# Optimization experiments

Measured on AMD Instinct MI355X. Metric: run time of the kernel, lower is better.

## Reference

```python
import jax, jax.numpy as jnp
import numpy as np

NV, C, ED, V, D, KS = 14, 2, 32, 3, 16, 3   # num_vars, codebook, embed_dim, views, depth, kernel
K_STATES = C ** NV                          # 16384 combinatorial states
B = 32


def _all_idcs():
    # itertools.product(range(C), repeat=NV) order: first variable varies slowest
    s = np.arange(K_STATES)
    pw = C ** np.arange(NV - 1, -1, -1)
    return (s[:, None] // pw[None, :]) % C  # (K, NV) int


def _convT(h, w, b):
    # torch ConvTranspose2d (stride=1, pad=0) == full conv with spatially-flipped kernel, in/out swapped
    wt = jnp.transpose(jnp.flip(w, (2, 3)), (1, 0, 2, 3))  # (out,in,k,k)
    y = jax.lax.conv_general_dilated(h, wt, (1, 1), [(KS - 1, KS - 1)] * 2,
                                     dimension_numbers=('NCHW', 'OIHW', 'NCHW'))
    return y + b[None, :, None, None]


def _decoder(z_flat, lw, lb, w1, b1, w2, b2, w3, b3):
    h = (z_flat @ lw + lb).reshape(-1, 4 * D, 1, 1)          # (K, 64, 1, 1)
    h = jax.nn.elu(_convT(h, w1, b1))                        # (K, 32, 3, 3)
    h = jax.nn.elu(_convT(h, w2, b2))                        # (K, 16, 5, 5)
    h = _convT(h, w3, b3)                                    # (K, 1, 7, 7)
    return h[:, 0]                                           # (K, 7, 7)


def setup_inputs() -> dict:
    key = jax.random.key(0)
    ks = jax.random.split(key, 6)
    sc = jnp.float32(0.05)
    return {
        'x': jax.random.normal(ks[0], (B, V, 7, 7), jnp.float32),
        'latent_embedding': jax.random.normal(ks[1], (NV, C, ED), jnp.float32),
        'lin_w': jax.random.normal(ks[2], (V, NV * ED, 4 * D), jnp.float32) * sc,
        'lin_b': jnp.zeros((V, 4 * D), jnp.float32),
        'w1': jax.random.normal(ks[3], (V, 4 * D, 2 * D, KS, KS), jnp.float32) * sc,
        'b1': jnp.zeros((V, 2 * D), jnp.float32),
        'w2': jax.random.normal(ks[4], (V, 2 * D, D, KS, KS), jnp.float32) * sc,
        'b2': jnp.zeros((V, D), jnp.float32),
        'w3': jax.random.normal(ks[5], (V, D, 1, KS, KS), jnp.float32) * sc,
        'b3': jnp.zeros((V, 1), jnp.float32),
    }


def reference(x, latent_embedding, lin_w, lin_b, w1, b1, w2, b2, w3, b3):
    idcs = jnp.asarray(_all_idcs())                                   # (K, NV) const
    z = latent_embedding[jnp.arange(NV)[None, :], idcs]               # (K, NV, ED)
    zf = z.reshape(K_STATES, NV * ED)
    means = jax.vmap(_decoder, in_axes=(None, 0, 0, 0, 0, 0, 0, 0, 0))(
        zf, lin_w, lin_b, w1, b1, w2, b2, w3, b3)                     # (V, K, 7, 7)
    means = jnp.transpose(means, (1, 0, 2, 3))                        # (K, V, 7, 7)
    # obs_logits: -0.5 * sum((means[None] - x[:, None])**2) over (h, w)
    return -0.5 * jnp.sum((means[None] - x[:, None]) ** 2, axis=(-2, -1))  # (B, K, V)
```

## Files before the change

kernel.cpp:

```cpp
#include <hip/hip_runtime.h>
#include <math.h>

#define NVARS 14
#define EDIM 32
#define VMIX 3
#define KSTATES 16384
#define BATCH 32

#define WS_DSWZ_B  32768
#define WS_W2SWZ_B (WS_DSWZ_B + 55296)
#define WS_W3SWZ_B (WS_W2SWZ_B + 718848)

#define H1S 296
#define H2S 420
#define MS  72

typedef __attribute__((ext_vector_type(8))) short bf16x8;
typedef __attribute__((ext_vector_type(4))) float f32x4;
typedef __attribute__((ext_vector_type(2))) unsigned int u32x2;

static __device__ inline unsigned short f2bf(float f) {
    unsigned u = __float_as_uint(f);
    u += 0x7FFFu + ((u >> 16) & 1u);
    return (unsigned short)(u >> 16);
}
static __device__ inline unsigned cvtpk(float lo, float hi) {
    unsigned r;
    asm("v_cvt_pk_bf16_f32 %0, %1, %2" : "=v"(r) : "v"(lo), "v"(hi));
    return r;
}
static __device__ inline float elu(float x) {
    return x > 0.f ? x : (__expf(x) - 1.f);
}

__global__ __launch_bounds__(320) void pre_kernel(const float* __restrict__ emb,
                                                  const float* __restrict__ lin_w,
                                                  const float* __restrict__ lin_b,
                                                  const float* __restrict__ b1,
                                                  const float* __restrict__ w1,
                                                  const float* __restrict__ w2,
                                                  const float* __restrict__ w3,
                                                  float* __restrict__ ws) {
    int blk = blockIdx.x;
    int tid = threadIdx.x;
    char* wsb = (char*)ws;
    unsigned short* dmat = (unsigned short*)(wsb + WS_DSWZ_B);
    __shared__ float sP[128];
    __shared__ float sQ[64];

    if (blk < 172) {
        int g2 = blk * 320 + tid;
        if (g2 >= 54912) return;
        bf16x8 o8;
        if (g2 < 44928) {
            int h = g2;
            int v = h / 14976;
            int r = h % 14976;
            int kt = r / 1664;
            int r2 = r % 1664;
            int nt = r2 / 64, l = r2 % 64;
            int n = nt * 16 + (l & 15);
            int kbase = kt * 32 + ((l >> 4) & 3) * 8;
            #pragma unroll
            for (int j = 0; j < 8; ++j) {
                int k = kbase + j;
                float val = 0.f;
                if (n < 400) {
                    int i = k / 9, p = k % 9;
                    int py = p / 3, px = p % 3;
                    int o = n / 25, q = n % 25;
                    int qy = q / 5, qx = q % 5;
                    int ty = qy - py, tx = qx - px;
                    if (ty >= 0 && ty < 3 && tx >= 0 && tx < 3)
                        val = w2[((size_t)(v * 32 + i) * 16 + o) * 9 + ty * 3 + tx];
                }
                o8[j] = (short)f2bf(val);
            }
        } else {
            int h = g2 - 44928;
            int v = h / 3328;
            int r = h % 3328;
            int kt = r / 256;
            int r2 = r % 256;
            int nt = r2 / 64, l = r2 % 64;
            int n = nt * 16 + (l & 15);
            int kbase = kt * 32 + ((l >> 4) & 3) * 8;
            #pragma unroll
            for (int j = 0; j < 8; ++j) {
                int k = kbase + j;
                float val = 0.f;
                if (k < 400 && n < 49) {
                    int o = k / 25, q = k % 25;
                    int qy = q / 5, qx = q % 5;
                    int py = n / 7, px = n % 7;
                    int ty = py - qy, tx = px - qx;
                    if (ty >= 0 && ty < 3 && tx >= 0 && tx < 3)
                        val = w3[(size_t)(v * 16 + o) * 9 + ty * 3 + tx];
                }
                o8[j] = (short)f2bf(val);
            }
        }
        *(bf16x8*)(wsb + WS_DSWZ_B + ((size_t)g2 + 3456) * 16) = o8;
        return;
    }

    if (blk < 214) {
        int b = blk - 172;
        int v = b / 14;
        int k = b % 14;
        if (tid < 128) {
            int c = tid >> 6, i = tid & 63;
            const float* e = emb + (k * 2 + c) * EDIM;
            const float* lw = lin_w + ((size_t)v * 448 + k * 32) * 64 + i;
            float a0 = 0.f, a1 = 0.f;
            #pragma unroll
            for (int e2 = 0; e2 < 32; e2 += 2) {
                a0 = fmaf(e[e2], lw[e2 * 64], a0);
                a1 = fmaf(e[e2 + 1], lw[(e2 + 1) * 64], a1);
            }
            sP[tid] = a0 + a1;
        }
        __syncthreads();
        if (tid < 64) sQ[tid] = sP[64 + tid] - sP[tid];
        __syncthreads();
        if (tid < 288) {
            int n = tid;
            const float* w1v = w1 + (size_t)v * 64 * 288 + n;
            float a0 = 0.f, a1 = 0.f;
            #pragma unroll
            for (int i = 0; i < 64; i += 2) {
                a0 = fmaf(sQ[i], w1v[i * 288], a0);
                a1 = fmaf(sQ[i + 1], w1v[(i + 1) * 288], a1);
            }
            int nt = n >> 4;
            int l = (n & 15) | ((k >> 3) << 4);
            dmat[((size_t)(v * 18 + nt) * 64 + l) * 8 + (k & 7)] = f2bf(a0 + a1);
        }
        return;
    }

    {
        int v = blk - 214;
        for (int t = tid; t < 9216; t += 320) {
            int j3 = t & 7;
            int l = (t >> 3) & 63;
            int k2 = ((l >> 4) << 3) | j3;
            if (k2 >= 15) dmat[(size_t)v * 9216 + t] = 0;
        }
        if (tid < 128) {
            int half = tid >> 6, i = tid & 63;
            float a0 = 0.f, a1 = 0.f;
            for (int n2 = half * 7; n2 < half * 7 + 7; ++n2) {
                const float* e = emb + (n2 * 2) * EDIM;
                const float* lw = lin_w + ((size_t)v * 448 + n2 * 32) * 64 + i;
                #pragma unroll
                for (int e2 = 0; e2 < 32; e2 += 2) {
                    a0 = fmaf(e[e2], lw[e2 * 64], a0);
                    a1 = fmaf(e[e2 + 1], lw[(e2 + 1) * 64], a1);
                }
            }
            sP[tid] = a0 + a1;
        }
        __syncthreads();
        if (tid < 64) sQ[tid] = lin_b[v * 64 + tid] + sP[tid] + sP[64 + tid];
        __syncthreads();
        if (tid < 288) {
            int n = tid;
            const float* w1v = w1 + (size_t)v * 64 * 288 + n;
            float a0 = b1[v * 32 + n / 9], a1 = 0.f;
            #pragma unroll
            for (int i = 0; i < 64; i += 2) {
                a0 = fmaf(sQ[i], w1v[i * 288], a0);
                a1 = fmaf(sQ[i + 1], w1v[(i + 1) * 288], a1);
            }
            int nt = n >> 4;
            int l = (n & 15) | 16;
            dmat[((size_t)(v * 18 + nt) * 64 + l) * 8 + 6] = f2bf(a0 + a1);
        }
    }
}

__global__ __launch_bounds__(512, 4) void emission_main(const float* __restrict__ x,
                                                        const float* __restrict__ b2,
                                                        const float* __restrict__ b3p,
                                                        const float* __restrict__ ws,
                                                        float* __restrict__ out) {
    int bid = blockIdx.x;
    int group = bid / 24;
    int j24 = bid % 24;
    int v = j24 >> 3;
    int chunk = group * 8 + (j24 & 7);
    int tid = threadIdx.x;
    int w = tid >> 6;
    int l = tid & 63;
    int quad = l >> 4;
    int lc = l & 15;
    const char* wsb = (const char*)ws;

    __shared__ __align__(16) unsigned short uni[64 * H2S];
    __shared__ float sMsq[64];
    __shared__ float sXsq[32];
    __shared__ float sB2[16];

    if (tid < 16) sB2[tid] = b2[v * 16 + tid];
    if (tid < 64) sMsq[tid] = 0.f;
    if (tid >= 64 && tid < 96) {
        int b = tid - 64;
        const float* xb = x + (size_t)(b * 3 + v) * 49;
        float s = 0.f;
        #pragma unroll
        for (int p = 0; p < 49; ++p) s = fmaf(xb[p], xb[p], s);
        sXsq[b] = s;
    }

    int mt0 = w & 3;
    {
        int nh = w >> 2;
        int sg = chunk * 64 + mt0 * 16 + lc;
        bf16x8 abits;
        #pragma unroll
        for (int j = 0; j < 8; ++j) {
            int k = quad * 8 + j;
            unsigned short u = 0;
            if (k < 14) u = ((sg >> (13 - k)) & 1) ? 0x3F80 : 0;
            else if (k == 14) u = 0x3F80;
            abits[j] = (short)u;
        }
        const bf16x8* dsw = (const bf16x8*)(wsb + WS_DSWZ_B) + (size_t)v * 18 * 64;
        #pragma unroll 3
        for (int i = 0; i < 9; ++i) {
            int nt = nh * 9 + i;
            bf16x8 afrag = dsw[nt * 64 + l];
            f32x4 d = {0.f, 0.f, 0.f, 0.f};
            d = __builtin_amdgcn_mfma_f32_16x16x32_bf16(afrag, abits, d, 0, 0, 0);
            unsigned lo = cvtpk(elu(d[0]), elu(d[1]));
            unsigned hi = cvtpk(elu(d[2]), elu(d[3]));
            *(u32x2*)&uni[(mt0 * 16 + lc) * H1S + nt * 16 + quad * 4] = (u32x2){lo, hi};
        }
    }
    __syncthreads();

    int ncnt = (w == 0) ? 4 : 3;
    int n0 = (w == 0) ? 0 : 1 + 3 * w;
    f32x4 acc[4][4];
    #pragma unroll
    for (int mt = 0; mt < 4; ++mt)
        #pragma unroll
        for (int j = 0; j < 4; ++j)
            acc[mt][j] = (f32x4){0.f, 0.f, 0.f, 0.f};
    {
        const bf16x8* w2f = (const bf16x8*)(wsb + WS_W2SWZ_B) + (size_t)v * 9 * 26 * 64;
        for (int kt = 0; kt < 9; ++kt) {
            bf16x8 af[4];
            #pragma unroll
            for (int j = 0; j < 4; ++j)
                if (j < ncnt) af[j] = w2f[(kt * 26 + n0 + j) * 64 + l];
            bf16x8 hb[4];
            #pragma unroll
            for (int mt = 0; mt < 4; ++mt)
                hb[mt] = *(const bf16x8*)&uni[(mt * 16 + lc) * H1S + kt * 32 + quad * 8];
            #pragma unroll
            for (int j = 0; j < 4; ++j)
                if (j < ncnt)
                    #pragma unroll
                    for (int mt = 0; mt < 4; ++mt)
                        acc[mt][j] = __builtin_amdgcn_mfma_f32_16x16x32_bf16(af[j], hb[mt], acc[mt][j], 0, 0, 0);
        }
    }
    __syncthreads();

    bf16x8 xf[2];
    {
        int bt = w >> 2;
        #pragma unroll
        for (int kt = 0; kt < 2; ++kt) {
            int b = bt * 16 + lc;
            const float* xb = x + (size_t)(b * 3 + v) * 49;
            union { bf16x8 h; unsigned u[4]; } xu;
            #pragma unroll
            for (int jj = 0; jj < 4; ++jj) {
                int p0 = kt * 32 + quad * 8 + jj * 2;
                float f0 = (p0 < 49) ? xb[p0] : 0.f;
                float f1 = (p0 + 1 < 49) ? xb[p0 + 1] : 0.f;
                xu.u[jj] = cvtpk(f0, f1);
            }
            xf[kt] = xu.h;
        }
    }

    #pragma unroll
    for (int j = 0; j < 4; ++j) {
        if (j < ncnt) {
            #pragma unroll
            for (int mt = 0; mt < 4; ++mt) {
                float vv[4];
                #pragma unroll
                for (int r = 0; r < 4; ++r) {
                    int n = (n0 + j) * 16 + quad * 4 + r;
                    vv[r] = elu(acc[mt][j][r] + sB2[n / 25]);
                }
                unsigned lo = cvtpk(vv[0], vv[1]);
                unsigned hi = cvtpk(vv[2], vv[3]);
                *(u32x2*)&uni[(mt * 16 + lc) * H2S + (n0 + j) * 16 + quad * 4] = (u32x2){lo, hi};
            }
        }
    }
    if (w == 1) {
        unsigned short* rowp = &uni[l * H2S + 400];
        *(u32x2*)&rowp[0]  = (u32x2){0u, 0u};
        *(u32x2*)&rowp[4]  = (u32x2){0u, 0u};
        *(u32x2*)&rowp[8]  = (u32x2){0u, 0u};
        *(u32x2*)&rowp[12] = (u32x2){0u, 0u};
    }
    __syncthreads();

    int ph = w >> 2;
    f32x4 acc2[2];
    acc2[0] = (f32x4){0.f, 0.f, 0.f, 0.f};
    acc2[1] = (f32x4){0.f, 0.f, 0.f, 0.f};
    {
        const bf16x8* w3f = (const bf16x8*)(wsb + WS_W3SWZ_B) + (size_t)v * 13 * 4 * 64;
        for (int kt = 0; kt < 13; ++kt) {
            bf16x8 hb = *(const bf16x8*)&uni[(mt0 * 16 + lc) * H2S + kt * 32 + quad * 8];
            #pragma unroll
            for (int c = 0; c < 2; ++c) {
                int pt = ph + 2 * c;
                bf16x8 af = w3f[(kt * 4 + pt) * 64 + l];
                acc2[c] = __builtin_amdgcn_mfma_f32_16x16x32_bf16(af, hb, acc2[c], 0, 0, 0);
            }
        }
    }
    float b3v = b3p[v];
    float mv[2][4];
    #pragma unroll
    for (int c = 0; c < 2; ++c) {
        #pragma unroll
        for (int r = 0; r < 4; ++r) {
            int p = (ph + 2 * c) * 16 + quad * 4 + r;
            mv[c][r] = (p < 49) ? (acc2[c][r] + b3v) : 0.f;
        }
    }
    {
        float sq = 0.f;
        #pragma unroll
        for (int c = 0; c < 2; ++c)
            #pragma unroll
            for (int r = 0; r < 4; ++r)
                sq = fmaf(mv[c][r], mv[c][r], sq);
        sq += __shfl_xor(sq, 16, 64);
        sq += __shfl_xor(sq, 32, 64);
        if (l < 16) atomicAdd(&sMsq[mt0 * 16 + lc], sq);
    }
    __syncthreads();
    #pragma unroll
    for (int c = 0; c < 2; ++c) {
        unsigned lo = cvtpk(mv[c][0], mv[c][1]);
        unsigned hi = cvtpk(mv[c][2], mv[c][3]);
        *(u32x2*)&uni[(mt0 * 16 + lc) * MS + (ph + 2 * c) * 16 + quad * 4] = (u32x2){lo, hi};
    }
    __syncthreads();

    {
        int st = w & 3, bt = w >> 2;
        f32x4 acc3 = {0.f, 0.f, 0.f, 0.f};
        #pragma unroll
        for (int kt = 0; kt < 2; ++kt) {
            bf16x8 bm = *(const bf16x8*)&uni[(st * 16 + lc) * MS + kt * 32 + quad * 8];
            acc3 = __builtin_amdgcn_mfma_f32_16x16x32_bf16(xf[kt], bm, acc3, 0, 0, 0);
        }
        int s = st * 16 + lc;
        float msq = sMsq[s];
        size_t kidx = (size_t)(chunk * 64 + s) * 3 + v;
        #pragma unroll
        for (int r = 0; r < 4; ++r) {
            int b = bt * 16 + quad * 4 + r;
            out[(size_t)b * (KSTATES * 3) + kidx] = acc3[r] - 0.5f * (msq + sXsq[b]);
        }
    }
}

extern "C" void kernel_launch(void* const* d_in, const int* in_sizes, int n_in,
                              void* d_out, int out_size, void* d_ws, size_t ws_size,
                              hipStream_t stream) {
    const float* x    = (const float*)d_in[0];
    const float* emb  = (const float*)d_in[1];
    const float* linw = (const float*)d_in[2];
    const float* linb = (const float*)d_in[3];
    const float* w1   = (const float*)d_in[4];
    const float* b1   = (const float*)d_in[5];
    const float* w2   = (const float*)d_in[6];
    const float* b2   = (const float*)d_in[7];
    const float* w3   = (const float*)d_in[8];
    const float* b3   = (const float*)d_in[9];
    float* out = (float*)d_out;
    float* ws = (float*)d_ws;

    pre_kernel<<<217, 320, 0, stream>>>(emb, linw, linb, b1, w1, w2, w3, ws);
    emission_main<<<768, 512, 0, stream>>>(x, b2, b3, ws, out);
}
```

Baseline: 104.7 us.

## Replace dense Toeplitz conv2 GEMM with sparse per-tap MFMA over compact weights

Conv2 is no longer run as a dense GEMM against a zero-padded Toeplitz matrix. Each wave now handles a set of output positions listed in QPACK and accumulates only the valid 3x3 taps, reading a compact per-tap 32x16 weight block. The h1 layout becomes position-major and the h2 layout output-position-major to match, and the w3 matrix is regenerated for the new ordering. The aim is to cut the redundant zero MFMAs and the large weight workspace reads. In exchange it adds data-dependent loops, uneven work across waves, and more LDS reads per MFMA.

New measurement: 103.0 us. About the same (-1.6%).

```diff
diff --git a/kernel.cpp b/kernel.cpp
--- a/kernel.cpp
+++ b/kernel.cpp
@@ -8,8 +8,8 @@
 #define BATCH 32
 
 #define WS_DSWZ_B  32768
-#define WS_W2SWZ_B (WS_DSWZ_B + 55296)
-#define WS_W3SWZ_B (WS_W2SWZ_B + 718848)
+#define WS_W2C_B   (WS_DSWZ_B + 55296)
+#define WS_W3SWZ_B (WS_W2C_B + 27648)
 
 #define H1S 296
 #define H2S 420
@@ -32,6 +32,17 @@
 static __device__ inline float elu(float x) {
     return x > 0.f ? x : (__expf(x) - 1.f);
 }
+
+static __device__ const unsigned QPACK[8] = {
+    0xFF04000Cu,
+    0xFF140607u,
+    0xFF18080Bu,
+    0xFFFF100Du,
+    0xFFFF1211u,
+    0x03010E0Au,
+    0x09051602u,
+    0x1715130Fu
+};
 
 __global__ __launch_bounds__(320) void pre_kernel(const float* __restrict__ emb,
                                                   const float* __restrict__ lin_w,
@@ -48,49 +59,23 @@
     __shared__ float sP[128];
     __shared__ float sQ[64];
 
-    if (blk < 172) {
+    if (blk < 37) {
         int g2 = blk * 320 + tid;
-        if (g2 >= 54912) return;
-        bf16x8 o8;
-        if (g2 < 44928) {
-            int h = g2;
-            int v = h / 14976;
-            int r = h % 14976;
-            int kt = r / 1664;
-            int r2 = r % 1664;
-            int nt = r2 / 64, l = r2 % 64;
-            int n = nt * 16 + (l & 15);
-            int kbase = kt * 32 + ((l >> 4) & 3) * 8;
-            #pragma unroll
-            for (int j = 0; j < 8; ++j) {
-                int k = kbase + j;
-                float val = 0.f;
-                if (n < 400) {
-                    int i = k / 9, p = k % 9;
-                    int py = p / 3, px = p % 3;
-                    int o = n / 25, q = n % 25;
-                    int qy = q / 5, qx = q % 5;
-                    int ty = qy - py, tx = qx - px;
-                    if (ty >= 0 && ty < 3 && tx >= 0 && tx < 3)
-                        val = w2[((size_t)(v * 32 + i) * 16 + o) * 9 + ty * 3 + tx];
-                }
-                o8[j] = (short)f2bf(val);
-            }
-        } else {
-            int h = g2 - 44928;
-            int v = h / 3328;
-            int r = h % 3328;
+        if (g2 < 9984) {
+            int v = g2 / 3328;
+            int r = g2 % 3328;
             int kt = r / 256;
             int r2 = r % 256;
             int nt = r2 / 64, l = r2 % 64;
             int n = nt * 16 + (l & 15);
             int kbase = kt * 32 + ((l >> 4) & 3) * 8;
+            bf16x8 o8;
             #pragma unroll
             for (int j = 0; j < 8; ++j) {
                 int k = kbase + j;
                 float val = 0.f;
                 if (k < 400 && n < 49) {
-                    int o = k / 25, q = k % 25;
+                    int q = k >> 4, o = k & 15;
                     int qy = q / 5, qx = q % 5;
                     int py = n / 7, px = n % 7;
                     int ty = py - qy, tx = px - qx;
@@ -99,13 +84,27 @@
                 }
                 o8[j] = (short)f2bf(val);
             }
-        }
-        *(bf16x8*)(wsb + WS_DSWZ_B + ((size_t)g2 + 3456) * 16) = o8;
+            *(bf16x8*)(wsb + WS_W3SWZ_B + (size_t)g2 * 16) = o8;
+        } else if (g2 < 11712) {
+            int g = g2 - 9984;
+            int v = g / 576;
+            int r = g % 576;
+            int t = r / 64, l = r % 64;
+            int o = l & 15;
+            int ibase = ((l >> 4) & 3) * 8;
+            bf16x8 o8;
+            #pragma unroll
+            for (int j = 0; j < 8; ++j) {
+                int i = ibase + j;
+                o8[j] = (short)f2bf(w2[((size_t)(v * 32 + i) * 16 + o) * 9 + t]);
+            }
+            *(bf16x8*)(wsb + WS_W2C_B + (size_t)g * 16) = o8;
+        }
         return;
     }
 
-    if (blk < 214) {
-        int b = blk - 172;
+    if (blk < 79) {
+        int b = blk - 37;
         int v = b / 14;
         int k = b % 14;
         if (tid < 128) {
@@ -132,15 +131,17 @@
                 a0 = fmaf(sQ[i], w1v[i * 288], a0);
                 a1 = fmaf(sQ[i + 1], w1v[(i + 1) * 288], a1);
             }
-            int nt = n >> 4;
-            int l = (n & 15) | ((k >> 3) << 4);
+            int ci = n / 9, p = n % 9;
+            int n2 = p * 32 + ci;
+            int nt = n2 >> 4;
+            int l = (n2 & 15) | ((k >> 3) << 4);
             dmat[((size_t)(v * 18 + nt) * 64 + l) * 8 + (k & 7)] = f2bf(a0 + a1);
         }
         return;
     }
 
     {
-        int v = blk - 214;
+        int v = blk - 79;
         for (int t = tid; t < 9216; t += 320) {
             int j3 = t & 7;
             int l = (t >> 3) & 63;
@@ -173,8 +174,10 @@
                 a0 = fmaf(sQ[i], w1v[i * 288], a0);
                 a1 = fmaf(sQ[i + 1], w1v[(i + 1) * 288], a1);
             }
-            int nt = n >> 4;
-            int l = (n & 15) | 16;
+            int ci = n / 9, p = n % 9;
+            int n2 = p * 32 + ci;
+            int nt = n2 >> 4;
+            int l = (n2 & 15) | 16;
             dmat[((size_t)(v * 18 + nt) * 64 + l) * 8 + 6] = f2bf(a0 + a1);
         }
     }
@@ -240,31 +243,35 @@
     }
     __syncthreads();
 
-    int ncnt = (w == 0) ? 4 : 3;
-    int n0 = (w == 0) ? 0 : 1 + 3 * w;
     f32x4 acc[4][4];
     #pragma unroll
-    for (int mt = 0; mt < 4; ++mt)
-        #pragma unroll
-        for (int j = 0; j < 4; ++j)
-            acc[mt][j] = (f32x4){0.f, 0.f, 0.f, 0.f};
-    {
-        const bf16x8* w2f = (const bf16x8*)(wsb + WS_W2SWZ_B) + (size_t)v * 9 * 26 * 64;
-        for (int kt = 0; kt < 9; ++kt) {
-            bf16x8 af[4];
-            #pragma unroll
-            for (int j = 0; j < 4; ++j)
-                if (j < ncnt) af[j] = w2f[(kt * 26 + n0 + j) * 64 + l];
-            bf16x8 hb[4];
-            #pragma unroll
-            for (int mt = 0; mt < 4; ++mt)
-                hb[mt] = *(const bf16x8*)&uni[(mt * 16 + lc) * H1S + kt * 32 + quad * 8];
-            #pragma unroll
-            for (int j = 0; j < 4; ++j)
-                if (j < ncnt)
-                    #pragma unroll
-                    for (int mt = 0; mt < 4; ++mt)
-                        acc[mt][j] = __builtin_amdgcn_mfma_f32_16x16x32_bf16(af[j], hb[mt], acc[mt][j], 0, 0, 0);
+    for (int ti = 0; ti < 4; ++ti)
+        #pragma unroll
+        for (int mt = 0; mt < 4; ++mt)
+            acc[ti][mt] = (f32x4){0.f, 0.f, 0.f, 0.f};
+    {
+        const bf16x8* w2c = (const bf16x8*)(wsb + WS_W2C_B) + (size_t)v * 9 * 64;
+        unsigned qp = QPACK[w];
+        #pragma unroll
+        for (int ti = 0; ti < 4; ++ti) {
+            int q = (qp >> (8 * ti)) & 255;
+            if (q != 255) {
+                int qy = q / 5, qx = q % 5;
+                int py0 = qy > 2 ? qy - 2 : 0, py1 = qy < 2 ? qy : 2;
+                int px0 = qx > 2 ? qx - 2 : 0, px1 = qx < 2 ? qx : 2;
+                for (int py = py0; py <= py1; ++py) {
+                    for (int px = px0; px <= px1; ++px) {
+                        int p = py * 3 + px;
+                        int t = (qy - py) * 3 + (qx - px);
+                        bf16x8 af = w2c[t * 64 + l];
+                        #pragma unroll
+                        for (int mt = 0; mt < 4; ++mt) {
+                            bf16x8 hb = *(const bf16x8*)&uni[(mt * 16 + lc) * H1S + p * 32 + quad * 8];
+                            acc[ti][mt] = __builtin_amdgcn_mfma_f32_16x16x32_bf16(af, hb, acc[ti][mt], 0, 0, 0);
+                        }
+                    }
+                }
+            }
         }
     }
     __syncthreads();
@@ -288,20 +295,22 @@
         }
     }
 
-    #pragma unroll
-    for (int j = 0; j < 4; ++j) {
-        if (j < ncnt) {
-            #pragma unroll
-            for (int mt = 0; mt < 4; ++mt) {
-                float vv[4];
+    {
+        unsigned qp = QPACK[w];
+        #pragma unroll
+        for (int ti = 0; ti < 4; ++ti) {
+            int q = (qp >> (8 * ti)) & 255;
+            if (q != 255) {
                 #pragma unroll
-                for (int r = 0; r < 4; ++r) {
-                    int n = (n0 + j) * 16 + quad * 4 + r;
-                    vv[r] = elu(acc[mt][j][r] + sB2[n / 25]);
+                for (int mt = 0; mt < 4; ++mt) {
+                    float vv[4];
+                    #pragma unroll
+                    for (int r = 0; r < 4; ++r)
+                        vv[r] = elu(acc[ti][mt][r] + sB2[quad * 4 + r]);
+                    unsigned lo = cvtpk(vv[0], vv[1]);
+                    unsigned hi = cvtpk(vv[2], vv[3]);
+                    *(u32x2*)&uni[(mt * 16 + lc) * H2S + q * 16 + quad * 4] = (u32x2){lo, hi};
                 }
-                unsigned lo = cvtpk(vv[0], vv[1]);
-                unsigned hi = cvtpk(vv[2], vv[3]);
-                *(u32x2*)&uni[(mt * 16 + lc) * H2S + (n0 + j) * 16 + quad * 4] = (u32x2){lo, hi};
             }
         }
     }
@@ -395,6 +404,6 @@
     float* out = (float*)d_out;
     float* ws = (float*)d_ws;
 
-    pre_kernel<<<217, 320, 0, stream>>>(emb, linw, linb, b1, w1, w2, w3, ws);
+    pre_kernel<<<82, 320, 0, stream>>>(emb, linw, linb, b1, w1, w2, w3, ws);
     emission_main<<<768, 512, 0, stream>>>(x, b2, b3, ws, out);
 }
```
